# Performance work log

Hardware: AMD Instinct MI355X
Metric: run time of the kernel (lower is better)

The kernel has to match this reference:

```python
import jax, jax.numpy as jnp
import numpy as np


def _seg(data, ids, n):
    return jax.ops.segment_sum(data, ids, num_segments=n)


def _cheb_lap_weights(src, dst, ew, n):
    # PyG ChebConv norm: L = I - D^-1/2 A D^-1/2, scaled L_hat = 2L/lambda_max - I.
    # With default lambda_max=2.0 the diagonal of L_hat is 0 and off-diagonal is -norm.
    deg = _seg(ew, src, n)
    dinv = jnp.where(deg > 0, deg ** -0.5, 0.0)
    return -(dinv[src] * ew * dinv[dst])  # [E]


def _cheb_apply(x, w_lap, src, dst, n, W, b):
    # Chebyshev recursion: Tx0=x, Tx1=L x, Tx_k = 2 L Tx_{k-1} - Tx_{k-2}
    def L(v):
        return _seg(w_lap[:, None] * v[src], dst, n)
    Tx0 = x
    Tx1 = L(x)
    out = Tx0 @ W[0] + Tx1 @ W[1]
    for k in range(2, W.shape[0]):
        Tx2 = 2.0 * L(Tx1) - Tx0
        out = out + Tx2 @ W[k]
        Tx0, Tx1 = Tx1, Tx2
    return out + b


def _gcn(x, src, dst, ew, n, W, b):
    # PyG GCNConv: add self-loops (weight 1), sym norm D~^-1/2 (A+I) D~^-1/2, x@W first.
    deg = _seg(ew, dst, n) + 1.0
    dinv = jnp.where(deg > 0, deg ** -0.5, 0.0)
    xw = x @ W
    norm = dinv[src] * ew * dinv[dst]
    out = _seg(norm[:, None] * xw[src], dst, n) + (dinv * dinv)[:, None] * xw
    return out + b


def setup_inputs() -> dict:
    key = jax.random.key(0)
    ks = jax.random.split(key, 16)
    num_nodes, B, T = 64, 256, 64
    hid, out_ch, ncls = 64, 64, 4
    epg = num_nodes * 16  # edges per graph (avg degree 16)
    N = num_nodes * B
    E = epg * B
    off = (jnp.arange(B, dtype=jnp.int64) * num_nodes)[:, None]
    src = (jax.random.randint(ks[0], (B, epg), 0, num_nodes) + off).reshape(-1)
    dst = (jax.random.randint(ks[1], (B, epg), 0, num_nodes) + off).reshape(-1)
    return {
        "x": jax.random.normal(ks[2], (N, T), jnp.float32),
        "edge_weight": jax.random.uniform(ks[3], (E,), jnp.float32, 0.1, 1.0),
        "wA": jax.random.normal(ks[4], (4, 1, hid), jnp.float32) * 0.1,
        "bA": jax.random.normal(ks[5], (hid,), jnp.float32) * 0.1,
        "wB": jax.random.normal(ks[6], (4, hid, hid), jnp.float32) * 0.1,
        "bB": jax.random.normal(ks[7], (hid,), jnp.float32) * 0.1,
        "w1": jax.random.normal(ks[8], (hid, out_ch), jnp.float32) * 0.1,
        "b1": jax.random.normal(ks[9], (out_ch,), jnp.float32) * 0.1,
        "w2": jax.random.normal(ks[10], (out_ch, out_ch // 2), jnp.float32) * 0.1,
        "b2": jax.random.normal(ks[11], (out_ch // 2,), jnp.float32) * 0.1,
        "wfc": jax.random.normal(ks[12], (num_nodes * out_ch // 2, ncls), jnp.float32) * 0.1,
        "bfc": jax.random.normal(ks[13], (ncls,), jnp.float32) * 0.1,
        "edge_src": src.astype(jnp.int64),
        "edge_dst": dst.astype(jnp.int64),
        "num_nodes": 64,
    }


def reference(x, edge_weight, wA, bA, wB, bB, w1, b1, w2, b2, wfc, bfc, edge_src, edge_dst, num_nodes):
    N = x.shape[0]
    B = N // num_nodes
    w_lap = _cheb_lap_weights(edge_src, edge_dst, edge_weight, N)

    def step(h, xt):  # xt: [N]
        a = _cheb_apply(xt[:, None], w_lap, edge_src, edge_dst, N, wA, bA)
        bh = _cheb_apply(h, w_lap, edge_src, edge_dst, N, wB, bB)
        h_new = jax.nn.sigmoid(a + bh)
        return h_new, None

    h0 = jnp.zeros((N, wB.shape[1]), x.dtype)
    h, _ = jax.lax.scan(step, h0, x.T)  # loop over T; only last h is used downstream

    z = jax.nn.relu(_gcn(h, edge_src, edge_dst, edge_weight, N, w1, b1))
    z = jax.nn.relu(_gcn(z, edge_src, edge_dst, edge_weight, N, w2, b2))
    z = z.reshape(B, -1)  # [B, num_nodes * out_ch/2]
    return jax.nn.log_softmax(z @ wfc + bfc, axis=1)
```

## Files before the change

kernel.cpp:

```cpp
#include <hip/hip_runtime.h>
#include <math.h>

#define NODES 64
#define NSTEPS 64
#define EPG 1024
#define NTHREADS 512
#define NBLOCKS 256

typedef _Float16 f16;
typedef f16 f16x8 __attribute__((ext_vector_type(8)));
typedef f16 f16x4 __attribute__((ext_vector_type(4)));
typedef float f32x4 __attribute__((ext_vector_type(4)));

#define OFF_M1    0
#define OFF_YF    0
#define OFF_M2    9216
#define OFF_M3    18432
#define OFF_M1T   27648
#define OFF_HF    27648
#define OFF_M2T   36864
#define OFF_HTF   36864
#define OFF_XT    46080
#define OFF_ZT    55296
#define OFF_WT    88064
#define OFF_LGF   126976
#define OFF_DEG   143360
#define OFF_DINV  143616
#define OFF_BSUM  143872
#define OFF_LOGIT 144128
#define SMEM_BYTES 144384

__device__ __forceinline__ f32x4 mfma16(f16x8 a, f16x8 b, f32x4 c) {
  return __builtin_amdgcn_mfma_f32_16x16x32_f16(a, b, c, 0, 0, 0);
}

#if __has_builtin(__builtin_amdgcn_mfma_f32_16x16x16f16)
#define HAVE_MFMA_K16 1
__device__ __forceinline__ f32x4 mfma16k16(f16x4 a, f16x4 b, f32x4 c) {
  return __builtin_amdgcn_mfma_f32_16x16x16f16(a, b, c, 0, 0, 0);
}
#else
#define HAVE_MFMA_K16 0
#endif

__device__ __forceinline__ f32x4 mm64t(const f16* __restrict__ A, const f16* __restrict__ B,
                                       int rb, int cb, int lrow, int lk)
{
  f32x4 d = (f32x4){0.f, 0.f, 0.f, 0.f};
#pragma unroll
  for (int ch = 0; ch < 2; ++ch) {
    const f16x8 a = *(const f16x8*)(A + (rb * 16 + lrow) * 72 + ch * 32 + lk * 8);
    const f16x8 b = *(const f16x8*)(B + (cb * 16 + lrow) * 72 + ch * 32 + lk * 8);
    d = mfma16(a, b, d);
  }
  return d;
}

template<int K>
__device__ __forceinline__ void mm4x4_acc(float acc[4][4],
                                          const float* __restrict__ A, int lda, int arow,
                                          const float* __restrict__ Bm, int ldb, int j4)
{
#pragma unroll 2
  for (int kc = 0; kc < K; kc += 4) {
    float av[4][4];
    float bv[4][4];
#pragma unroll
    for (int rr = 0; rr < 4; ++rr) {
      const float4 t = *(const float4*)(A + (arow + rr) * lda + kc);
      av[rr][0] = t.x; av[rr][1] = t.y; av[rr][2] = t.z; av[rr][3] = t.w;
    }
#pragma unroll
    for (int kk = 0; kk < 4; ++kk) {
      const float4 t = *(const float4*)(Bm + (kc + kk) * ldb + j4);
      bv[kk][0] = t.x; bv[kk][1] = t.y; bv[kk][2] = t.z; bv[kk][3] = t.w;
    }
#pragma unroll
    for (int rr = 0; rr < 4; ++rr)
#pragma unroll
      for (int cc = 0; cc < 4; ++cc) {
        float s = acc[rr][cc];
#pragma unroll
        for (int kk = 0; kk < 4; ++kk) s += av[rr][kk] * bv[kk][cc];
        acc[rr][cc] = s;
      }
  }
}

__global__ __launch_bounds__(NTHREADS, 2)
void gcrnn_mfma4(const float* __restrict__ x,
                 const float* __restrict__ ew,
                 const float* __restrict__ wA,
                 const float* __restrict__ bA,
                 const float* __restrict__ wB,
                 const float* __restrict__ bB,
                 const float* __restrict__ w1,
                 const float* __restrict__ b1,
                 const float* __restrict__ w2,
                 const float* __restrict__ b2,
                 const float* __restrict__ wfc,
                 const float* __restrict__ bfc,
                 const int* __restrict__ esrc,
                 const int* __restrict__ edst,
                 float* __restrict__ out)
{
  __shared__ __align__(16) char smem[SMEM_BYTES];

  f16*   sM1   = (f16*)(smem + OFF_M1);
  f16*   sM2   = (f16*)(smem + OFF_M2);
  f16*   sM3   = (f16*)(smem + OFF_M3);
  f16*   sM1T  = (f16*)(smem + OFF_M1T);
  f16*   sM2T  = (f16*)(smem + OFF_M2T);
  f16*   sXT   = (f16*)(smem + OFF_XT);
  f16*   sZt   = (f16*)(smem + OFF_ZT);
  f16*   sWt   = (f16*)(smem + OFF_WT);
  float* sLgF  = (float*)(smem + OFF_LGF);
  float* sDeg  = (float*)(smem + OFF_DEG);
  float* sDinv = (float*)(smem + OFF_DINV);
  float* sBsum = (float*)(smem + OFF_BSUM);
  float* sLogit= (float*)(smem + OFF_LOGIT);

  const int b = blockIdx.x, tid = threadIdx.x;
  const int gbase = b * NODES, ebase = b * EPG;
  const int wid = tid >> 6, lane = tid & 63;
  const int lrow = lane & 15, lk = lane >> 4;
  const bool isA = wid < 4;
  const int fb = wid;
  const int nb = wid & 3;

  for (int idx = tid; idx < 4096; idx += NTHREADS) sLgF[idx] = 0.f;
  if (tid < 64) { sDeg[tid] = 0.f; sBsum[tid] = bA[tid] + bB[tid]; }
  for (int idx = tid; idx < 64 * 260; idx += NTHREADS) {
    const int k = idx >> 6, c = idx & 63;
    const float v = (k < 256) ? wB[(k >> 6) * 4096 + (k & 63) * 64 + c]
                              : wA[(k - 256) * 64 + c];
    sWt[c * 304 + k] = (f16)v;
  }
  for (int idx = tid; idx < 64 * 44; idx += NTHREADS) {
    const int c = idx / 44, j = idx - c * 44;
    sWt[c * 304 + 260 + j] = (f16)0.f;
  }
  for (int idx = tid; idx < 4096; idx += NTHREADS) {
    const int n = idx >> 6, t = idx & 63;
    sXT[t * 72 + n] = (f16)x[gbase * 64 + idx];
  }
  __syncthreads();

  for (int e = tid; e < EPG; e += NTHREADS)
    atomicAdd(&sDeg[esrc[ebase + e] - gbase], ew[ebase + e]);
  __syncthreads();
  if (tid < 64) { const float d = sDeg[tid]; sDinv[tid] = (d > 0.f) ? rsqrtf(d) : 0.f; }
  __syncthreads();
  for (int e = tid; e < EPG; e += NTHREADS) {
    const int sl = esrc[ebase + e] - gbase, dl = edst[ebase + e] - gbase;
    atomicAdd(&sLgF[dl * 64 + sl], -(sDinv[sl] * ew[ebase + e] * sDinv[dl]));
  }
  __syncthreads();
  for (int idx = tid; idx < 4096; idx += NTHREADS) {
    const int i = idx >> 6, j = idx & 63;
    const f16 v = (f16)sLgF[idx];
    sM1[i * 72 + j] = v;
    sM1T[j * 72 + i] = v;
  }
  __syncthreads();

  const int rbS = wid >> 1;

#pragma unroll
  for (int s = 0; s < 2; ++s) {
    const int cbS = (wid & 1) * 2 + s;
    f32x4 d;
    d = mm64t(sM1T, sM1, rbS, cbS, lrow, lk);
    {
      const int p0 = rbS * 16 + lk * 4, q = cbS * 16 + lrow;
      f16x4 w;
#pragma unroll
      for (int r = 0; r < 4; ++r) w[r] = (f16)(2.f * d[r] - ((p0 + r) == q ? 1.f : 0.f));
      *(f16x4*)(sM2 + q * 72 + p0) = w;
    }
    d = mm64t(sM1, sM1T, rbS, cbS, lrow, lk);
    {
      const int p0 = rbS * 16 + lk * 4, q = cbS * 16 + lrow;
      f16x4 w;
#pragma unroll
      for (int r = 0; r < 4; ++r) w[r] = (f16)(2.f * d[r] - ((p0 + r) == q ? 1.f : 0.f));
      *(f16x4*)(sM2T + q * 72 + p0) = w;
    }
    d = mm64t(sM1, sXT, rbS, cbS, lrow, lk);
    {
      const int p0 = rbS * 16 + lk * 4, q = cbS * 16 + lrow;
#pragma unroll
      for (int r = 0; r < 4; ++r) sZt[q * 256 + (p0 + r) * 4 + 1] = (f16)d[r];
    }
  }
  for (int idx = tid; idx < 4096; idx += NTHREADS) {
    const int t = idx >> 6, n = idx & 63;
    sZt[t * 256 + n * 4 + 0] = sXT[t * 72 + n];
  }
  __syncthreads();

#pragma unroll
  for (int s = 0; s < 2; ++s) {
    const int cbS = (wid & 1) * 2 + s;
    f32x4 d;
    d = mm64t(sM2T, sM1, rbS, cbS, lrow, lk);
    {
      const int p0 = rbS * 16 + lk * 4, q = cbS * 16 + lrow;
      const f16x4 lv = *(const f16x4*)(sM1 + q * 72 + p0);
      f16x4 w;
#pragma unroll
      for (int r = 0; r < 4; ++r) w[r] = (f16)(2.f * d[r] - (float)lv[r]);
      *(f16x4*)(sM3 + q * 72 + p0) = w;
    }
    d = mm64t(sM2, sXT, rbS, cbS, lrow, lk);
    {
      const int p0 = rbS * 16 + lk * 4, q = cbS * 16 + lrow;
#pragma unroll
      for (int r = 0; r < 4; ++r) sZt[q * 256 + (p0 + r) * 4 + 2] = (f16)d[r];
    }
  }
  __syncthreads();

#pragma unroll
  for (int s = 0; s < 2; ++s) {
    const int cbS = (wid & 1) * 2 + s;
    f32x4 d = mm64t(sM3, sXT, rbS, cbS, lrow, lk);
    const int p0 = rbS * 16 + lk * 4, q = cbS * 16 + lrow;
#pragma unroll
    for (int r = 0; r < 4; ++r) sZt[q * 256 + (p0 + r) * 4 + 3] = (f16)d[r];
  }
  __syncthreads();

  f16x8 frag[36];
  float bsrv[4];
  f16x4 iF;
#pragma unroll
  for (int e = 0; e < 4; ++e) iF[e] = (f16)((lrow == lk * 4 + e) ? 1.f : 0.f);

  if (isA) {
#pragma unroll
    for (int k = 0; k < 3; ++k)
#pragma unroll
      for (int nn = 0; nn < 4; ++nn)
#pragma unroll
        for (int ch = 0; ch < 2; ++ch)
          frag[(k * 4 + nn) * 2 + ch] =
            *(const f16x8*)((const f16*)(smem + OFF_M1 + k * 9216) + (nn * 16 + lrow) * 72 + ch * 32 + lk * 8);
  } else {
#pragma unroll
    for (int cb = 0; cb < 4; ++cb) {
#pragma unroll
      for (int j = 0; j < 9; ++j)
        frag[cb * 9 + j] = *(const f16x8*)(sWt + (cb * 16 + lrow) * 304 + j * 32 + lk * 8);
      bsrv[cb] = sBsum[cb * 16 + lrow];
    }
  }
  for (int idx = tid; idx < 2048; idx += NTHREADS) {
    ((int*)(smem + OFF_HF))[idx] = 0;
    ((int*)(smem + OFF_HTF))[idx] = 0;
  }
  __syncthreads();

#pragma unroll 1
  for (int t = 0; t < NSTEPS; ++t) {
    f32x4 p0v, p1v, p2v, p3v;
    if (isA) {
      const f16x8 aT0 = *(const f16x8*)(smem + OFF_HTF + (fb * 2 + 0) * 1024 + lane * 16);
      const f16x8 aT1 = *(const f16x8*)(smem + OFF_HTF + (fb * 2 + 1) * 1024 + lane * 16);
      const int lslot = (lrow + 16 * ((fb & 1) * 2 + (lk >> 1))) * 16 + (lk & 1) * 8;
#pragma unroll
      for (int k = 0; k < 3; ++k)
#pragma unroll
        for (int nn = 0; nn < 4; ++nn) {
          f32x4 d = (f32x4){0.f, 0.f, 0.f, 0.f};
          d = mfma16(aT0, frag[(k * 4 + nn) * 2 + 0], d);
          d = mfma16(aT1, frag[(k * 4 + nn) * 2 + 1], d);
          f16x4 w;
#pragma unroll
          for (int r = 0; r < 4; ++r) w[r] = (f16)d[r];
          *(f16x4*)(smem + OFF_YF + (((k * 4 + nn) * 2 + (fb >> 1)) * 1024) + lslot) = w;
        }
    } else {
      const f16x8 ah0 = *(const f16x8*)(smem + OFF_HF + (nb * 2 + 0) * 1024 + lane * 16);
      const f16x8 ah1 = *(const f16x8*)(smem + OFF_HF + (nb * 2 + 1) * 1024 + lane * 16);
      const f16x4 zv = *(const f16x4*)(smem + OFF_ZT + t * 512 + (nb * 16 + lrow) * 8);
      f16x8 az;
      az[0] = zv[0]; az[1] = zv[1]; az[2] = zv[2]; az[3] = zv[3];
      az[4] = (f16)0.f; az[5] = (f16)0.f; az[6] = (f16)0.f; az[7] = (f16)0.f;
      p0v = (f32x4){bsrv[0], bsrv[0], bsrv[0], bsrv[0]};
      p1v = (f32x4){bsrv[1], bsrv[1], bsrv[1], bsrv[1]};
      p2v = (f32x4){bsrv[2], bsrv[2], bsrv[2], bsrv[2]};
      p3v = (f32x4){bsrv[3], bsrv[3], bsrv[3], bsrv[3]};
      p0v = mfma16(ah0, frag[0 * 9 + 0], p0v); p0v = mfma16(ah1, frag[0 * 9 + 1], p0v); p0v = mfma16(az, frag[0 * 9 + 8], p0v);
      p1v = mfma16(ah0, frag[1 * 9 + 0], p1v); p1v = mfma16(ah1, frag[1 * 9 + 1], p1v); p1v = mfma16(az, frag[1 * 9 + 8], p1v);
      p2v = mfma16(ah0, frag[2 * 9 + 0], p2v); p2v = mfma16(ah1, frag[2 * 9 + 1], p2v); p2v = mfma16(az, frag[2 * 9 + 8], p2v);
      p3v = mfma16(ah0, frag[3 * 9 + 0], p3v); p3v = mfma16(ah1, frag[3 * 9 + 1], p3v); p3v = mfma16(az, frag[3 * 9 + 8], p3v);
    }
    __syncthreads();

    if (!isA) {
#pragma unroll
      for (int k = 0; k < 3; ++k)
#pragma unroll
        for (int ch = 0; ch < 2; ++ch) {
          const f16x8 ay = *(const f16x8*)(smem + OFF_YF + (((k * 4 + nb) * 2 + ch) * 1024) + lane * 16);
          const int j = 2 + 2 * k + ch;
          p0v = mfma16(ay, frag[0 * 9 + j], p0v);
          p1v = mfma16(ay, frag[1 * 9 + j], p1v);
          p2v = mfma16(ay, frag[2 * 9 + j], p2v);
          p3v = mfma16(ay, frag[3 * 9 + j], p3v);
        }
#pragma unroll
      for (int cb = 0; cb < 4; ++cb) {
        const f32x4 pv = (cb == 0) ? p0v : (cb == 1) ? p1v : (cb == 2) ? p2v : p3v;
        f16x4 hv;
#pragma unroll
        for (int r = 0; r < 4; ++r) hv[r] = (f16)(1.f / (1.f + __expf(-pv[r])));
        *(f16x4*)(smem + OFF_HTF + ((cb * 2 + (nb >> 1)) * 64 + lrow + 16 * ((nb & 1) * 2 + (lk >> 1))) * 16 + (lk & 1) * 8) = hv;
#if HAVE_MFMA_K16
        f32x4 d2 = mfma16k16(hv, iF, (f32x4){0.f, 0.f, 0.f, 0.f});
        f16x4 h2;
#pragma unroll
        for (int r = 0; r < 4; ++r) h2[r] = (f16)d2[r];
        *(f16x4*)(smem + OFF_HF + ((nb * 2 + (cb >> 1)) * 64 + lrow + 16 * ((cb & 1) * 2 + (lk >> 1))) * 16 + (lk & 1) * 8) = h2;
#else
#pragma unroll
        for (int r = 0; r < 4; ++r)
          ((f16*)(smem + OFF_HF))[((nb * 2 + (cb >> 1)) * 64 + (lk * 4 + r) + 16 * ((cb & 1) * 2 + (lrow >> 3))) * 8 + (lrow & 7)] = hv[r];
#endif
      }
    }
    __syncthreads();
  }

  float* sLgG = (float*)(smem + OFF_ZT);
  float* sT1g = (float*)(smem + OFF_WT);
  float* sT2g = (float*)(smem + OFF_WT + 17408);
  const f16* hF = (const f16*)(smem + OFF_HF);

  for (int idx = tid; idx < 64 * 68; idx += NTHREADS) sLgG[idx] = 0.f;
  if (tid < 64) sDeg[tid] = 0.f;
  for (int idx = tid; idx < 4096; idx += NTHREADS) {
    const int n = idx >> 6, c = idx & 63;
    const f16 v = hF[(((n >> 4) * 2 + (c >> 5)) * 64 + (n & 15) + 16 * ((c >> 3) & 3)) * 8 + (c & 7)];
    sT1g[n * 68 + c] = (float)v;
  }
  if (tid < 4) sLogit[tid] = bfc[tid];
  __syncthreads();
  for (int e = tid; e < EPG; e += NTHREADS)
    atomicAdd(&sDeg[edst[ebase + e] - gbase], ew[ebase + e]);
  __syncthreads();
  if (tid < 64) sDinv[tid] = rsqrtf(sDeg[tid] + 1.f);
  __syncthreads();
  for (int e = tid; e < EPG; e += NTHREADS) {
    const int sl = esrc[ebase + e] - gbase, dl = edst[ebase + e] - gbase;
    atomicAdd(&sLgG[dl * 68 + sl], sDinv[sl] * ew[ebase + e] * sDinv[dl]);
  }
  __syncthreads();
  if (tid < 64) sLgG[tid * 68 + tid] += sDinv[tid] * sDinv[tid];
  __syncthreads();

  const bool isTile = tid < 256;
  const int i4 = ((tid >> 4) & 15) * 4;
  const int j4 = (tid & 15) * 4;

  if (isTile) {
    float m[4][4] = {};
    mm4x4_acc<64>(m, sT1g, 68, i4, w1, 64, j4);
#pragma unroll
    for (int rr = 0; rr < 4; ++rr)
      *(float4*)(sT2g + (i4 + rr) * 68 + j4) = make_float4(m[rr][0], m[rr][1], m[rr][2], m[rr][3]);
  }
  __syncthreads();
  if (isTile) {
    float m[4][4] = {};
    mm4x4_acc<64>(m, sLgG, 68, i4, sT2g, 68, j4);
#pragma unroll
    for (int rr = 0; rr < 4; ++rr) {
      float4 o;
      o.x = fmaxf(m[rr][0] + b1[j4 + 0], 0.f);
      o.y = fmaxf(m[rr][1] + b1[j4 + 1], 0.f);
      o.z = fmaxf(m[rr][2] + b1[j4 + 2], 0.f);
      o.w = fmaxf(m[rr][3] + b1[j4 + 3], 0.f);
      *(float4*)(sT1g + (i4 + rr) * 68 + j4) = o;
    }
  }
  __syncthreads();
  if (isTile && j4 < 32) {
    float m[4][4] = {};
    mm4x4_acc<64>(m, sT1g, 68, i4, w2, 32, j4);
#pragma unroll
    for (int rr = 0; rr < 4; ++rr)
      *(float4*)(sT2g + (i4 + rr) * 68 + j4) = make_float4(m[rr][0], m[rr][1], m[rr][2], m[rr][3]);
  }
  __syncthreads();
  if (isTile && j4 < 32) {
    float m[4][4] = {};
    mm4x4_acc<64>(m, sLgG, 68, i4, sT2g, 68, j4);
#pragma unroll
    for (int rr = 0; rr < 4; ++rr) {
      float4 o;
      o.x = fmaxf(m[rr][0] + b2[j4 + 0], 0.f);
      o.y = fmaxf(m[rr][1] + b2[j4 + 1], 0.f);
      o.z = fmaxf(m[rr][2] + b2[j4 + 2], 0.f);
      o.w = fmaxf(m[rr][3] + b2[j4 + 3], 0.f);
      *(float4*)(sT1g + (i4 + rr) * 68 + j4) = o;
    }
  }
  __syncthreads();

  float q0 = 0.f, q1 = 0.f, q2 = 0.f, q3 = 0.f;
  for (int f = tid; f < 2048; f += NTHREADS) {
    const int n = f >> 5, c = f & 31;
    const float v = sT1g[n * 68 + c];
    const float4 wv = *(const float4*)(wfc + f * 4);
    q0 += v * wv.x; q1 += v * wv.y; q2 += v * wv.z; q3 += v * wv.w;
  }
#pragma unroll
  for (int off = 1; off < 64; off <<= 1) {
    q0 += __shfl_xor(q0, off);
    q1 += __shfl_xor(q1, off);
    q2 += __shfl_xor(q2, off);
    q3 += __shfl_xor(q3, off);
  }
  if ((tid & 63) == 0) {
    atomicAdd(&sLogit[0], q0);
    atomicAdd(&sLogit[1], q1);
    atomicAdd(&sLogit[2], q2);
    atomicAdd(&sLogit[3], q3);
  }
  __syncthreads();
  if (tid == 0) {
    const float l0 = sLogit[0], l1 = sLogit[1], l2 = sLogit[2], l3 = sLogit[3];
    const float mx = fmaxf(fmaxf(l0, l1), fmaxf(l2, l3));
    const float s = expf(l0 - mx) + expf(l1 - mx) + expf(l2 - mx) + expf(l3 - mx);
    const float lse = mx + logf(s);
    out[b * 4 + 0] = l0 - lse;
    out[b * 4 + 1] = l1 - lse;
    out[b * 4 + 2] = l2 - lse;
    out[b * 4 + 3] = l3 - lse;
  }
}

extern "C" void kernel_launch(void* const* d_in, const int* in_sizes, int n_in,
                              void* d_out, int out_size, void* d_ws, size_t ws_size,
                              hipStream_t stream) {
  gcrnn_mfma4<<<NBLOCKS, NTHREADS, 0, stream>>>(
      (const float*)d_in[0],
      (const float*)d_in[1],
      (const float*)d_in[2],
      (const float*)d_in[3],
      (const float*)d_in[4],
      (const float*)d_in[5],
      (const float*)d_in[6],
      (const float*)d_in[7],
      (const float*)d_in[8],
      (const float*)d_in[9],
      (const float*)d_in[10],
      (const float*)d_in[11],
      (const int*)d_in[12],
      (const int*)d_in[13],
      (float*)d_out);
}
```

Before: 111.8 us.

## Merge A/B warp roles into uniform 4-wave blocks with double-buffered hidden state

Shrinks the block from 8 to 4 wavefronts. Each wave now does both the Chebyshev propagation (L^k h) and the weight projection for its own 16-node row block, instead of splitting those across two wave groups. Per-wave Y scratch plus double-buffered h/hT removes one of the two block barriers per time step and eliminates the cross-wave Y handoff. The cost is more serial MFMA work per wave, fewer waves per CU to hide latency, and larger register footprint from keeping both the W and M fragments resident.

```diff
diff --git a/kernel.cpp b/kernel.cpp
--- a/kernel.cpp
+++ b/kernel.cpp
@@ -4,7 +4,7 @@
 #define NODES 64
 #define NSTEPS 64
 #define EPG 1024
-#define NTHREADS 512
+#define NTHREADS 256
 #define NBLOCKS 256
 
 typedef _Float16 f16;
@@ -12,22 +12,16 @@
 typedef f16 f16x4 __attribute__((ext_vector_type(4)));
 typedef float f32x4 __attribute__((ext_vector_type(4)));
 
-#define OFF_M1    0
-#define OFF_YF    0
-#define OFF_M2    9216
-#define OFF_M3    18432
-#define OFF_M1T   27648
-#define OFF_HF    27648
-#define OFF_M2T   36864
-#define OFF_HTF   36864
-#define OFF_XT    46080
-#define OFF_ZT    55296
-#define OFF_WT    88064
-#define OFF_LGF   126976
-#define OFF_DEG   143360
-#define OFF_DINV  143616
-#define OFF_BSUM  143872
-#define OFF_LOGIT 144128
+#define R_WZ    0
+#define R_M     38912
+#define R_MT    66560
+#define R_H     84992
+#define R_XT    117760
+#define R_LGF   126976
+#define R_DEG   143360
+#define R_DINV  143616
+#define R_BSUM  143872
+#define R_LOGIT 144128
 #define SMEM_BYTES 144384
 
 __device__ __forceinline__ f32x4 mfma16(f16x8 a, f16x8 b, f32x4 c) {
@@ -87,8 +81,8 @@
   }
 }
 
-__global__ __launch_bounds__(NTHREADS, 2)
-void gcrnn_mfma4(const float* __restrict__ x,
+__global__ __launch_bounds__(NTHREADS, 1)
+void gcrnn_mfma5(const float* __restrict__ x,
                  const float* __restrict__ ew,
                  const float* __restrict__ wA,
                  const float* __restrict__ bA,
@@ -106,27 +100,24 @@
 {
   __shared__ __align__(16) char smem[SMEM_BYTES];
 
-  f16*   sM1   = (f16*)(smem + OFF_M1);
-  f16*   sM2   = (f16*)(smem + OFF_M2);
-  f16*   sM3   = (f16*)(smem + OFF_M3);
-  f16*   sM1T  = (f16*)(smem + OFF_M1T);
-  f16*   sM2T  = (f16*)(smem + OFF_M2T);
-  f16*   sXT   = (f16*)(smem + OFF_XT);
-  f16*   sZt   = (f16*)(smem + OFF_ZT);
-  f16*   sWt   = (f16*)(smem + OFF_WT);
-  float* sLgF  = (float*)(smem + OFF_LGF);
-  float* sDeg  = (float*)(smem + OFF_DEG);
-  float* sDinv = (float*)(smem + OFF_DINV);
-  float* sBsum = (float*)(smem + OFF_BSUM);
-  float* sLogit= (float*)(smem + OFF_LOGIT);
+  f16*   sWt   = (f16*)(smem + R_WZ);
+  f16*   sZt   = (f16*)(smem + R_WZ);
+  f16*   sM1   = (f16*)(smem + R_M);
+  f16*   sM2   = (f16*)(smem + R_M + 9216);
+  f16*   sM3   = (f16*)(smem + R_M + 18432);
+  f16*   sM1T  = (f16*)(smem + R_MT);
+  f16*   sM2T  = (f16*)(smem + R_MT + 9216);
+  f16*   sXT   = (f16*)(smem + R_XT);
+  float* sLgF  = (float*)(smem + R_LGF);
+  float* sDeg  = (float*)(smem + R_DEG);
+  float* sDinv = (float*)(smem + R_DINV);
+  float* sBsum = (float*)(smem + R_BSUM);
+  float* sLogit= (float*)(smem + R_LOGIT);
 
   const int b = blockIdx.x, tid = threadIdx.x;
   const int gbase = b * NODES, ebase = b * EPG;
   const int wid = tid >> 6, lane = tid & 63;
   const int lrow = lane & 15, lk = lane >> 4;
-  const bool isA = wid < 4;
-  const int fb = wid;
-  const int nb = wid & 3;
 
   for (int idx = tid; idx < 4096; idx += NTHREADS) sLgF[idx] = 0.f;
   if (tid < 64) { sDeg[tid] = 0.f; sBsum[tid] = bA[tid] + bB[tid]; }
@@ -156,65 +147,71 @@
     atomicAdd(&sLgF[dl * 64 + sl], -(sDinv[sl] * ew[ebase + e] * sDinv[dl]));
   }
   __syncthreads();
+
+  f16x8 Wfrag[4][9];
+  float bsrv[4];
   for (int idx = tid; idx < 4096; idx += NTHREADS) {
     const int i = idx >> 6, j = idx & 63;
     const f16 v = (f16)sLgF[idx];
     sM1[i * 72 + j] = v;
     sM1T[j * 72 + i] = v;
   }
-  __syncthreads();
-
-  const int rbS = wid >> 1;
-
-#pragma unroll
-  for (int s = 0; s < 2; ++s) {
-    const int cbS = (wid & 1) * 2 + s;
+#pragma unroll
+  for (int cb = 0; cb < 4; ++cb) {
+#pragma unroll
+    for (int j = 0; j < 9; ++j)
+      Wfrag[cb][j] = *(const f16x8*)(sWt + (cb * 16 + lrow) * 304 + j * 32 + lk * 8);
+    bsrv[cb] = sBsum[cb * 16 + lrow];
+  }
+  __syncthreads();
+
+#pragma unroll
+  for (int cbS = 0; cbS < 4; ++cbS) {
     f32x4 d;
-    d = mm64t(sM1T, sM1, rbS, cbS, lrow, lk);
-    {
-      const int p0 = rbS * 16 + lk * 4, q = cbS * 16 + lrow;
+    d = mm64t(sM1T, sM1, wid, cbS, lrow, lk);
+    {
+      const int p0 = wid * 16 + lk * 4, q = cbS * 16 + lrow;
       f16x4 w;
 #pragma unroll
       for (int r = 0; r < 4; ++r) w[r] = (f16)(2.f * d[r] - ((p0 + r) == q ? 1.f : 0.f));
       *(f16x4*)(sM2 + q * 72 + p0) = w;
     }
-    d = mm64t(sM1, sM1T, rbS, cbS, lrow, lk);
-    {
-      const int p0 = rbS * 16 + lk * 4, q = cbS * 16 + lrow;
+    d = mm64t(sM1, sM1T, wid, cbS, lrow, lk);
+    {
+      const int p0 = wid * 16 + lk * 4, q = cbS * 16 + lrow;
       f16x4 w;
 #pragma unroll
       for (int r = 0; r < 4; ++r) w[r] = (f16)(2.f * d[r] - ((p0 + r) == q ? 1.f : 0.f));
       *(f16x4*)(sM2T + q * 72 + p0) = w;
     }
-    d = mm64t(sM1, sXT, rbS, cbS, lrow, lk);
-    {
-      const int p0 = rbS * 16 + lk * 4, q = cbS * 16 + lrow;
+    d = mm64t(sM1, sXT, wid, cbS, lrow, lk);
+    {
+      const int p0 = wid * 16 + lk * 4, q = cbS * 16 + lrow;
 #pragma unroll
       for (int r = 0; r < 4; ++r) sZt[q * 256 + (p0 + r) * 4 + 1] = (f16)d[r];
     }
   }
   for (int idx = tid; idx < 4096; idx += NTHREADS) {
     const int t = idx >> 6, n = idx & 63;
-    sZt[t * 256 + n * 4 + 0] = sXT[t * 72 + n];
-  }
-  __syncthreads();
-
-#pragma unroll
-  for (int s = 0; s < 2; ++s) {
-    const int cbS = (wid & 1) * 2 + s;
+    sZt[(t * 64 + n) * 4 + 0] = sXT[t * 72 + n];
+  }
+  __syncthreads();
+
+#pragma unroll
+  for (int cbS = 0; cbS < 4; ++cbS) {
     f32x4 d;
-    d = mm64t(sM2T, sM1, rbS, cbS, lrow, lk);
-    {
-      const int p0 = rbS * 16 + lk * 4, q = cbS * 16 + lrow;
+    d = mm64t(sM2T, sM1, wid, cbS, lrow, lk);
+    {
+      const int p0 = wid * 16 + lk * 4, q = cbS * 16 + lrow;
       const f16x4 lv = *(const f16x4*)(sM1 + q * 72 + p0);
       f16x4 w;
 #pragma unroll
       for (int r = 0; r < 4; ++r) w[r] = (f16)(2.f * d[r] - (float)lv[r]);
       *(f16x4*)(sM3 + q * 72 + p0) = w;
     }
-    d = mm64t(sM2, sXT, rbS, cbS, lrow, lk);
-    {
-      const int p0 = rbS * 16 + lk * 4, q = cbS * 16 + lrow;
+    d = mm64t(sM2, sXT, wid, cbS, lrow, lk);
+    {
+      const int p0 = wid * 16 + lk * 4, q = cbS * 16 + lrow;
 #pragma unroll
       for (int r = 0; r < 4; ++r) sZt[q * 256 + (p0 + r) * 4 + 2] = (f16)d[r];
     }
@@ -222,121 +219,115 @@
   __syncthreads();
 
 #pragma unroll
-  for (int s = 0; s < 2; ++s) {
-    const int cbS = (wid & 1) * 2 + s;
-    f32x4 d = mm64t(sM3, sXT, rbS, cbS, lrow, lk);
-    const int p0 = rbS * 16 + lk * 4, q = cbS * 16 + lrow;
+  for (int cbS = 0; cbS < 4; ++cbS) {
+    f32x4 d = mm64t(sM3, sXT, wid, cbS, lrow, lk);
+    const int p0 = wid * 16 + lk * 4, q = cbS * 16 + lrow;
 #pragma unroll
     for (int r = 0; r < 4; ++r) sZt[q * 256 + (p0 + r) * 4 + 3] = (f16)d[r];
   }
   __syncthreads();
 
-  f16x8 frag[36];
-  float bsrv[4];
+  f16x8 Mfrag[3][2];
+#pragma unroll
+  for (int k = 0; k < 3; ++k)
+#pragma unroll
+    for (int ch = 0; ch < 2; ++ch)
+      Mfrag[k][ch] = *(const f16x8*)((const f16*)(smem + R_M + k * 9216) + (wid * 16 + lrow) * 72 + ch * 32 + lk * 8);
   f16x4 iF;
 #pragma unroll
   for (int e = 0; e < 4; ++e) iF[e] = (f16)((lrow == lk * 4 + e) ? 1.f : 0.f);
-
-  if (isA) {
-#pragma unroll
-    for (int k = 0; k < 3; ++k)
-#pragma unroll
-      for (int nn = 0; nn < 4; ++nn)
-#pragma unroll
-        for (int ch = 0; ch < 2; ++ch)
-          frag[(k * 4 + nn) * 2 + ch] =
-            *(const f16x8*)((const f16*)(smem + OFF_M1 + k * 9216) + (nn * 16 + lrow) * 72 + ch * 32 + lk * 8);
-  } else {
-#pragma unroll
-    for (int cb = 0; cb < 4; ++cb) {
-#pragma unroll
-      for (int j = 0; j < 9; ++j)
-        frag[cb * 9 + j] = *(const f16x8*)(sWt + (cb * 16 + lrow) * 304 + j * 32 + lk * 8);
-      bsrv[cb] = sBsum[cb * 16 + lrow];
-    }
-  }
-  for (int idx = tid; idx < 2048; idx += NTHREADS) {
-    ((int*)(smem + OFF_HF))[idx] = 0;
-    ((int*)(smem + OFF_HTF))[idx] = 0;
-  }
-  __syncthreads();
-
+  for (int idx = tid; idx < 4096; idx += NTHREADS)
+    ((int*)(smem + R_H))[idx] = 0;
+  __syncthreads();
+
+  char* const Yb = smem + R_M + wid * 6144;
 #pragma unroll 1
   for (int t = 0; t < NSTEPS; ++t) {
-    f32x4 p0v, p1v, p2v, p3v;
-    if (isA) {
-      const f16x8 aT0 = *(const f16x8*)(smem + OFF_HTF + (fb * 2 + 0) * 1024 + lane * 16);
-      const f16x8 aT1 = *(const f16x8*)(smem + OFF_HTF + (fb * 2 + 1) * 1024 + lane * 16);
-      const int lslot = (lrow + 16 * ((fb & 1) * 2 + (lk >> 1))) * 16 + (lk & 1) * 8;
-#pragma unroll
-      for (int k = 0; k < 3; ++k)
-#pragma unroll
-        for (int nn = 0; nn < 4; ++nn) {
-          f32x4 d = (f32x4){0.f, 0.f, 0.f, 0.f};
-          d = mfma16(aT0, frag[(k * 4 + nn) * 2 + 0], d);
-          d = mfma16(aT1, frag[(k * 4 + nn) * 2 + 1], d);
-          f16x4 w;
-#pragma unroll
-          for (int r = 0; r < 4; ++r) w[r] = (f16)d[r];
-          *(f16x4*)(smem + OFF_YF + (((k * 4 + nn) * 2 + (fb >> 1)) * 1024) + lslot) = w;
-        }
-    } else {
-      const f16x8 ah0 = *(const f16x8*)(smem + OFF_HF + (nb * 2 + 0) * 1024 + lane * 16);
-      const f16x8 ah1 = *(const f16x8*)(smem + OFF_HF + (nb * 2 + 1) * 1024 + lane * 16);
-      const f16x4 zv = *(const f16x4*)(smem + OFF_ZT + t * 512 + (nb * 16 + lrow) * 8);
-      f16x8 az;
+    const int cur = t & 1, nxt = cur ^ 1;
+    const char* hTc = smem + R_H + cur * 16384;
+    const char* hc  = smem + R_H + cur * 16384 + 8192;
+    char* hTn = smem + R_H + nxt * 16384;
+    char* hn  = smem + R_H + nxt * 16384 + 8192;
+
+    f16x8 bT[4][2];
+#pragma unroll
+    for (int jt = 0; jt < 4; ++jt)
+#pragma unroll
+      for (int ch = 0; ch < 2; ++ch)
+        bT[jt][ch] = *(const f16x8*)(hTc + ((jt * 2 + ch) * 64 + lane) * 16);
+
+#pragma unroll
+    for (int k = 0; k < 3; ++k)
+#pragma unroll
+      for (int ft = 0; ft < 4; ++ft) {
+        f32x4 d = mfma16(Mfrag[k][0], bT[ft][0], (f32x4){0.f, 0.f, 0.f, 0.f});
+        d = mfma16(Mfrag[k][1], bT[ft][1], d);
+        f16x4 yv;
+#pragma unroll
+        for (int r = 0; r < 4; ++r) yv[r] = (f16)d[r];
+#if HAVE_MFMA_K16
+        f32x4 dT = mfma16k16(yv, iF, (f32x4){0.f, 0.f, 0.f, 0.f});
+        f16x4 yt;
+#pragma unroll
+        for (int r = 0; r < 4; ++r) yt[r] = (f16)dT[r];
+        *(f16x4*)(Yb + ((k * 2 + (ft >> 1)) * 64 + lrow + 16 * ((ft & 1) * 2 + (lk >> 1))) * 16 + (lk & 1) * 8) = yt;
+#else
+#pragma unroll
+        for (int r = 0; r < 4; ++r)
+          ((f16*)Yb)[((k * 2 + (ft >> 1)) * 64 + (lk * 4 + r) + 16 * ((ft & 1) * 2 + (lrow >> 3))) * 8 + (lrow & 7)] = yv[r];
+#endif
+      }
+    asm volatile("s_waitcnt lgkmcnt(0)" ::: "memory");
+
+    const f16x8 a0 = *(const f16x8*)(hc + ((wid * 2 + 0) * 64 + lane) * 16);
+    const f16x8 a1 = *(const f16x8*)(hc + ((wid * 2 + 1) * 64 + lane) * 16);
+    f16x8 ayv[6];
+#pragma unroll
+    for (int g = 0; g < 6; ++g)
+      ayv[g] = *(const f16x8*)(Yb + (g * 64 + lane) * 16);
+    f16x8 az;
+    {
+      const f16x4 zv = *(const f16x4*)(smem + R_WZ + (t * 64 + wid * 16 + lrow) * 8);
       az[0] = zv[0]; az[1] = zv[1]; az[2] = zv[2]; az[3] = zv[3];
       az[4] = (f16)0.f; az[5] = (f16)0.f; az[6] = (f16)0.f; az[7] = (f16)0.f;
-      p0v = (f32x4){bsrv[0], bsrv[0], bsrv[0], bsrv[0]};
-      p1v = (f32x4){bsrv[1], bsrv[1], bsrv[1], bsrv[1]};
-      p2v = (f32x4){bsrv[2], bsrv[2], bsrv[2], bsrv[2]};
-      p3v = (f32x4){bsrv[3], bsrv[3], bsrv[3], bsrv[3]};
-      p0v = mfma16(ah0, frag[0 * 9 + 0], p0v); p0v = mfma16(ah1, frag[0 * 9 + 1], p0v); p0v = mfma16(az, frag[0 * 9 + 8], p0v);
-      p1v = mfma16(ah0, frag[1 * 9 + 0], p1v); p1v = mfma16(ah1, frag[1 * 9 + 1], p1v); p1v = mfma16(az, frag[1 * 9 + 8], p1v);
-      p2v = mfma16(ah0, frag[2 * 9 + 0], p2v); p2v = mfma16(ah1, frag[2 * 9 + 1], p2v); p2v = mfma16(az, frag[2 * 9 + 8], p2v);
-      p3v = mfma16(ah0, frag[3 * 9 + 0], p3v); p3v = mfma16(ah1, frag[3 * 9 + 1], p3v); p3v = mfma16(az, frag[3 * 9 + 8], p3v);
+    }
+    f32x4 acc[4];
+#pragma unroll
+    for (int cb = 0; cb < 4; ++cb) {
+      acc[cb] = (f32x4){bsrv[cb], bsrv[cb], bsrv[cb], bsrv[cb]};
+      acc[cb] = mfma16(a0, Wfrag[cb][0], acc[cb]);
+      acc[cb] = mfma16(a1, Wfrag[cb][1], acc[cb]);
+#pragma unroll
+      for (int g = 0; g < 6; ++g)
+        acc[cb] = mfma16(ayv[g], Wfrag[cb][2 + g], acc[cb]);
+      acc[cb] = mfma16(az, Wfrag[cb][8], acc[cb]);
+    }
+
+#pragma unroll
+    for (int cb = 0; cb < 4; ++cb) {
+      f16x4 hv;
+#pragma unroll
+      for (int r = 0; r < 4; ++r) hv[r] = (f16)(1.f / (1.f + __expf(-acc[cb][r])));
+      *(f16x4*)(hTn + ((cb * 2 + (wid >> 1)) * 64 + lrow + 16 * ((wid & 1) * 2 + (lk >> 1))) * 16 + (lk & 1) * 8) = hv;
+#if HAVE_MFMA_K16
+      f32x4 dT = mfma16k16(hv, iF, (f32x4){0.f, 0.f, 0.f, 0.f});
+      f16x4 h2;
+#pragma unroll
+      for (int r = 0; r < 4; ++r) h2[r] = (f16)dT[r];
+      *(f16x4*)(hn + ((wid * 2 + (cb >> 1)) * 64 + lrow + 16 * ((cb & 1) * 2 + (lk >> 1))) * 16 + (lk & 1) * 8) = h2;
+#else
+#pragma unroll
+      for (int r = 0; r < 4; ++r)
+        ((f16*)hn)[((wid * 2 + (cb >> 1)) * 64 + (lk * 4 + r) + 16 * ((cb & 1) * 2 + (lrow >> 3))) * 8 + (lrow & 7)] = hv[r];
+#endif
     }
     __syncthreads();
-
-    if (!isA) {
-#pragma unroll
-      for (int k = 0; k < 3; ++k)
-#pragma unroll
-        for (int ch = 0; ch < 2; ++ch) {
-          const f16x8 ay = *(const f16x8*)(smem + OFF_YF + (((k * 4 + nb) * 2 + ch) * 1024) + lane * 16);
-          const int j = 2 + 2 * k + ch;
-          p0v = mfma16(ay, frag[0 * 9 + j], p0v);
-          p1v = mfma16(ay, frag[1 * 9 + j], p1v);
-          p2v = mfma16(ay, frag[2 * 9 + j], p2v);
-          p3v = mfma16(ay, frag[3 * 9 + j], p3v);
-        }
-#pragma unroll
-      for (int cb = 0; cb < 4; ++cb) {
-        const f32x4 pv = (cb == 0) ? p0v : (cb == 1) ? p1v : (cb == 2) ? p2v : p3v;
-        f16x4 hv;
-#pragma unroll
-        for (int r = 0; r < 4; ++r) hv[r] = (f16)(1.f / (1.f + __expf(-pv[r])));
-        *(f16x4*)(smem + OFF_HTF + ((cb * 2 + (nb >> 1)) * 64 + lrow + 16 * ((nb & 1) * 2 + (lk >> 1))) * 16 + (lk & 1) * 8) = hv;
-#if HAVE_MFMA_K16
-        f32x4 d2 = mfma16k16(hv, iF, (f32x4){0.f, 0.f, 0.f, 0.f});
-        f16x4 h2;
-#pragma unroll
-        for (int r = 0; r < 4; ++r) h2[r] = (f16)d2[r];
-        *(f16x4*)(smem + OFF_HF + ((nb * 2 + (cb >> 1)) * 64 + lrow + 16 * ((cb & 1) * 2 + (lk >> 1))) * 16 + (lk & 1) * 8) = h2;
-#else
-#pragma unroll
-        for (int r = 0; r < 4; ++r)
-          ((f16*)(smem + OFF_HF))[((nb * 2 + (cb >> 1)) * 64 + (lk * 4 + r) + 16 * ((cb & 1) * 2 + (lrow >> 3))) * 8 + (lrow & 7)] = hv[r];
-#endif
-      }
-    }
-    __syncthreads();
-  }
-
-  float* sLgG = (float*)(smem + OFF_ZT);
-  float* sT1g = (float*)(smem + OFF_WT);
-  float* sT2g = (float*)(smem + OFF_WT + 17408);
-  const f16* hF = (const f16*)(smem + OFF_HF);
+  }
+
+  float* sLgG = (float*)(smem + 0);
+  float* sT1g = (float*)(smem + 17408);
+  float* sT2g = (float*)(smem + 34816);
+  const f16* hF = (const f16*)(smem + R_H + 8192);
 
   for (int idx = tid; idx < 64 * 68; idx += NTHREADS) sLgG[idx] = 0.f;
   if (tid < 64) sDeg[tid] = 0.f;
@@ -360,11 +351,10 @@
   if (tid < 64) sLgG[tid * 68 + tid] += sDinv[tid] * sDinv[tid];
   __syncthreads();
 
-  const bool isTile = tid < 256;
   const int i4 = ((tid >> 4) & 15) * 4;
   const int j4 = (tid & 15) * 4;
 
-  if (isTile) {
+  {
     float m[4][4] = {};
     mm4x4_acc<64>(m, sT1g, 68, i4, w1, 64, j4);
 #pragma unroll
@@ -372,7 +362,7 @@
       *(float4*)(sT2g + (i4 + rr) * 68 + j4) = make_float4(m[rr][0], m[rr][1], m[rr][2], m[rr][3]);
   }
   __syncthreads();
-  if (isTile) {
+  {
     float m[4][4] = {};
     mm4x4_acc<64>(m, sLgG, 68, i4, sT2g, 68, j4);
 #pragma unroll
@@ -386,7 +376,7 @@
     }
   }
   __syncthreads();
-  if (isTile && j4 < 32) {
+  if (j4 < 32) {
     float m[4][4] = {};
     mm4x4_acc<64>(m, sT1g, 68, i4, w2, 32, j4);
 #pragma unroll
@@ -394,7 +384,7 @@
       *(float4*)(sT2g + (i4 + rr) * 68 + j4) = make_float4(m[rr][0], m[rr][1], m[rr][2], m[rr][3]);
   }
   __syncthreads();
-  if (isTile && j4 < 32) {
+  if (j4 < 32) {
     float m[4][4] = {};
     mm4x4_acc<64>(m, sLgG, 68, i4, sT2g, 68, j4);
 #pragma unroll
@@ -445,7 +435,7 @@
 extern "C" void kernel_launch(void* const* d_in, const int* in_sizes, int n_in,
                               void* d_out, int out_size, void* d_ws, size_t ws_size,
                               hipStream_t stream) {
-  gcrnn_mfma4<<<NBLOCKS, NTHREADS, 0, stream>>>(
+  gcrnn_mfma5<<<NBLOCKS, NTHREADS, 0, stream>>>(
       (const float*)d_in[0],
       (const float*)d_in[1],
       (const float*)d_in[2],
```

Measured after the change: 156.1 us. +39.6%, slower.
